# Kernel optimization log

Hardware: AMD Instinct MI355X
Metric: run time of the kernel (lower is better)

## Reference

```python
import jax, jax.numpy as jnp
import numpy as np

B, N, H, HEADS, NBINS = 64, 256, 512, 8, 3
DK = H // HEADS
NEG = -1e12

def setup_inputs() -> dict:
    key = jax.random.key(0)
    ks = jax.random.split(key, 20)
    def lin(k, out_d, in_d):
        w = jax.random.normal(k, (out_d, in_d), jnp.float32) * (1.0 / np.sqrt(in_d))
        b = jnp.zeros((out_d,), jnp.float32)
        return w, b
    x = jax.random.normal(ks[0], (B, N, H), jnp.float32)
    dist = jax.random.uniform(ks[1], (B, N - 1, N - 1), jnp.float32, 0.0, 10.0)
    dist_bar = jnp.sort(jax.random.uniform(ks[2], (B, NBINS), jnp.float32, 1.0, 9.0), axis=-1)
    mask = jnp.ones((B, N, N), jnp.float32)
    Wq, bq = lin(ks[3], H, H)
    Wk, bk = lin(ks[4], H, H)
    Wv, bv = lin(ks[5], H, H)
    Wa = jnp.stack([lin(ks[6 + i], H, H)[0] for i in range(NBINS)])  # [NBINS,H,H]
    ba = jnp.zeros((NBINS, H), jnp.float32)
    Ws1, bs1 = lin(ks[10], H, NBINS * H)
    Ws2, bs2 = lin(ks[11], H, H)
    gamma = jnp.ones((H,), jnp.float32)
    beta = jnp.zeros((H,), jnp.float32)
    return dict(x=x, dist=dist, dist_bar=dist_bar, mask=mask, Wq=Wq, bq=bq, Wk=Wk, bk=bk,
                Wv=Wv, bv=bv, Wa=Wa, ba=ba, Ws1=Ws1, bs1=bs1, Ws2=Ws2, bs2=bs2,
                gamma=gamma, beta=beta)

def reference(x, dist, dist_bar, mask, Wq, bq, Wk, bk, Wv, bv, Wa, ba, Ws1, bs1, Ws2, bs2, gamma, beta):
    residual = x
    def proj(x, W, b):  # torch Linear: x @ W.T + b
        return jnp.einsum('bnd,od->bno', x, W) + b
    def heads(t):  # [B,N,H] -> [B,heads,N,dk]
        return t.reshape(B, N, HEADS, DK).transpose(0, 2, 1, 3)
    q, k, v = heads(proj(x, Wq, bq)), heads(proj(x, Wk, bk)), heads(proj(x, Wv, bv))
    scores = jnp.einsum('bhnd,bhmd->bhnm', q, k) / jnp.sqrt(jnp.float32(DK))  # [B,heads,N,N]
    # padding mask (shape [B,1,N,N] != scores shape -> masked_fill(mask==0))
    scores = jnp.where(mask[:, None] == 0, NEG, scores)
    # new_dist: super node row/col = 1, interior = dist
    new_dist = jnp.ones((B, 1, N, N), jnp.float32).at[:, :, 1:, 1:].set(dist[:, None])
    multi_out, attn_list = [], []
    for i in range(NBINS):
        cut = dist_bar[:, i][:, None, None, None]          # per-batch threshold
        dm = new_dist < cut                                 # [B,1,N,N]
        dm = dm.at[:, :, 0, :].set(True).at[:, :, :, 0].set(True)
        sd = jnp.where(dm, scores, NEG)
        attn = jax.nn.softmax(sd, axis=-1)                  # dropout: eval mode
        attn_list.append(attn)
        multi_out.append(jnp.einsum('bhnm,bhmd->bhnd', attn, v))
    x_cat = jnp.concatenate([
        jnp.einsum('bnd,od->bno', multi_out[i].transpose(0, 2, 1, 3).reshape(B, N, H), Wa[i]) + ba[i]
        for i in range(NBINS)], axis=-1)                    # [B,N,NBINS*H]
    h = jax.nn.silu(jnp.einsum('bnd,od->bno', x_cat, Ws1) + bs1)
    h = jnp.einsum('bnd,od->bno', h, Ws2) + bs2
    h = h + residual
    mu = jnp.mean(h, axis=-1, keepdims=True)
    var = jnp.var(h, axis=-1, keepdims=True)
    out = (h - mu) / jnp.sqrt(var + 1e-6) * gamma + beta
    return (out, jnp.stack(attn_list))
```

## Files before the change

### kernel.cpp

```cpp
#include <hip/hip_runtime.h>
#include <cstddef>

#define NEGV (-1e12f)


typedef __attribute__((ext_vector_type(4))) float f32x4;
typedef __attribute__((ext_vector_type(8))) __bf16 bf16x8;

__device__ __forceinline__ unsigned short f2bf(float f) {
  union { float f; unsigned u; } v; v.f = f;
  unsigned r = v.u + 0x7FFFu + ((v.u >> 16) & 1u);
  return (unsigned short)(r >> 16);
}

#define GLDS16(gp, lp)                                                      \
  __builtin_amdgcn_global_load_lds(                                         \
      (const __attribute__((address_space(1))) void*)(gp),                  \
      (__attribute__((address_space(3))) void*)(lp), 16, 0, 0)

__global__ __launch_bounds__(256) void msa_prep(
    const float* __restrict__ x, const float* __restrict__ Wq,
    const float* __restrict__ Wk, const float* __restrict__ Wv,
    const float* __restrict__ Ws2, const float* __restrict__ Ws1,
    const float* __restrict__ Wa, const float* __restrict__ bq,
    const float* __restrict__ bk, const float* __restrict__ bv,
    const float* __restrict__ ba, const float* __restrict__ bs1,
    const float* __restrict__ dist, const float* __restrict__ dist_bar,
    const float* __restrict__ maskg,
    unsigned short* __restrict__ xb, unsigned short* __restrict__ Wqkvb,
    unsigned short* __restrict__ Ws2b, unsigned short* __restrict__ Wcatb,
    float* __restrict__ bcomb, float* __restrict__ bqkv,
    unsigned long long* __restrict__ bits) {
  __shared__ float As[16][36];
  __shared__ float Bs[16][68];
  const int blk = blockIdx.x;
  const int tid = threadIdx.x;
  if (blk < 8192) {
    int i = blk * 256 + tid;
    float4 v = ((const float4*)x)[i];
    ushort4 o; o.x = f2bf(v.x); o.y = f2bf(v.y); o.z = f2bf(v.z); o.w = f2bf(v.w);
    ((ushort4*)xb)[i] = o;
    return;
  }
  if (blk < 8960) {
    int sel = (blk - 8192) >> 8;
    int i = ((blk - 8192) & 255) * 256 + tid;
    const float* src = (sel == 0) ? Wq : (sel == 1) ? Wk : Wv;
    unsigned short* dst = Wqkvb + (size_t)sel * 262144;
    float4 v = ((const float4*)src)[i];
    ushort4 o; o.x = f2bf(v.x); o.y = f2bf(v.y); o.z = f2bf(v.z); o.w = f2bf(v.w);
    ((ushort4*)dst)[i] = o;
    return;
  }
  if (blk < 9216) {
    int i = (blk - 8960) * 256 + tid;
    float4 v = ((const float4*)Ws2)[i];
    ushort4 o; o.x = f2bf(v.x); o.y = f2bf(v.y); o.z = f2bf(v.z); o.w = f2bf(v.w);
    ((ushort4*)Ws2b)[i] = o;
    return;
  }
  if (blk < 9600) {
    const int t = blk - 9216;
    const int i = t >> 7;
    const int rem = t & 127;
    const int ob = (rem >> 3) * 32, cb = (rem & 7) * 64;
    const int tx = tid & 15, ty = tid >> 4;
    float acc[2][4] = {};
    for (int kt = 0; kt < 512; kt += 16) {
      __syncthreads();
      if (tid < 128) {
        int o = tid >> 2, e4 = (tid & 3) * 4;
        float4 a4 = *(const float4*)&Ws1[(size_t)(ob + o) * 1536 + i * 512 + kt + e4];
        As[e4 + 0][o] = a4.x; As[e4 + 1][o] = a4.y;
        As[e4 + 2][o] = a4.z; As[e4 + 3][o] = a4.w;
      }
      {
        int e = tid & 15, c4 = (tid >> 4) * 4;
        float4 b4 = *(const float4*)&Wa[((size_t)i << 18) + (size_t)(kt + e) * 512 + cb + c4];
        *(float4*)&Bs[e][c4] = b4;
      }
      __syncthreads();
#pragma unroll
      for (int k = 0; k < 16; ++k) {
        float a0 = As[k][ty * 2], a1 = As[k][ty * 2 + 1];
        float bb[4];
        *(float4*)bb = *(const float4*)&Bs[k][tx * 4];
#pragma unroll
        for (int c = 0; c < 4; ++c) {
          acc[0][c] += a0 * bb[c];
          acc[1][c] += a1 * bb[c];
        }
      }
    }
#pragma unroll
    for (int rr = 0; rr < 2; ++rr)
#pragma unroll
      for (int c = 0; c < 4; ++c)
        Wcatb[(size_t)(ob + ty * 2 + rr) * 1536 + i * 512 + cb + tx * 4 + c] =
            f2bf(acc[rr][c]);
    return;
  }
  if (blk < 9728) {
    const int o = (blk - 9600) * 4 + (tid >> 6);
    const int lane = tid & 63;
    const float* row = Ws1 + (size_t)o * 1536;
    float s = 0.f;
#pragma unroll
    for (int c0 = 0; c0 < 1536; c0 += 256) {
      s += row[c0 + lane] * ba[c0 + lane];
      s += row[c0 + 64 + lane] * ba[c0 + 64 + lane];
      s += row[c0 + 128 + lane] * ba[c0 + 128 + lane];
      s += row[c0 + 192 + lane] * ba[c0 + 192 + lane];
    }
#pragma unroll
    for (int off = 32; off > 0; off >>= 1) s += __shfl_xor(s, off);
    if (lane == 0) bcomb[o] = bs1[o] + s;
    return;
  }
  if (blk < 9729) {
    for (int i = tid; i < 1536; i += 256)
      bqkv[i] = (i < 512) ? bq[i] : (i < 1024) ? bk[i - 512] : bv[i - 1024];
    return;
  }
  {
    const int gw = (blk - 9729) * 4 + (tid >> 6);
    const int lane = tid & 63;
    const int b = gw >> 8, row = gw & 255;
    const float cut0 = dist_bar[b * 3 + 0];
    const float cut1 = dist_bar[b * 3 + 1];
    const float cut2 = dist_bar[b * 3 + 2];
    const float* mrow = maskg + (size_t)b * 65536 + (size_t)row * 256;
    const int rj = (row == 0) ? 1 : row;
    const float* drow = dist + (size_t)b * 65025 + (size_t)(rj - 1) * 255;
    unsigned long long* out = bits + (size_t)gw * 12;
#pragma unroll
    for (int cc = 0; cc < 4; ++cc) {
      const int col = cc * 64 + lane;
      const int cj = (col == 0) ? 1 : col;
      float dv = drow[cj - 1];
      bool sup = (row == 0) || (col == 0);
      bool mk = (mrow[col] != 0.f);
      if (sup) dv = -1e30f;
      unsigned long long b0 = __ballot(mk && (dv < cut0));
      unsigned long long b1 = __ballot(mk && (dv < cut1));
      unsigned long long b2 = __ballot(mk && (dv < cut2));
      if (lane == 0) { out[cc] = b0; out[4 + cc] = b1; out[8 + cc] = b2; }
    }
  }
}

template <int ACT, int RES, int OBF, int BK, int SQ>
__global__ __launch_bounds__(256) void msa_gemm_mfma(
    const unsigned short* __restrict__ A, int lda,
    const unsigned short* __restrict__ W, int ldw,
    const float* __restrict__ bias, const float* __restrict__ resid,
    void* __restrict__ Cout, int ldc, int Kdim) {
  constexpr int KSUB = BK / 32;
  constexpr int RPC = BK / 8;
  constexpr int CPT = (128 * RPC) / 256;
  __shared__ __align__(16) unsigned short Asm_[2][128 * BK];
  __shared__ __align__(16) unsigned short Bsm_[2][128 * BK];
  const int tid = threadIdx.x;
  const int lane = tid & 63, wv = tid >> 6;
  const int m0 = blockIdx.x * 128, n0 = blockIdx.y * 128;
  const int wr = wv >> 1, wc = wv & 1;
  const int fr = lane & 15, fq = lane >> 4;
  f32x4 acc[4][4] = {};
  const unsigned short* Ag[CPT];
  const unsigned short* Wg[CPT];
#pragma unroll
  for (int i = 0; i < CPT; ++i) {
    int c = tid + i * 256;
    int row = c / RPC, j = c % RPC;
    Ag[i] = A + (size_t)(m0 + row) * lda + j * 8;
    Wg[i] = W + (size_t)(n0 + row) * ldw + j * 8;
  }
#pragma unroll
  for (int i = 0; i < CPT; ++i) {
    GLDS16(Ag[i], &Asm_[0][(tid + i * 256) * 8]);
    GLDS16(Wg[i], &Bsm_[0][(tid + i * 256) * 8]);
  }
  __syncthreads();
  int cur = 0;
  for (int kt = 0; kt < Kdim; kt += BK) {
    if (kt + BK < Kdim) {
      const int nx = cur ^ 1, k2 = kt + BK;
#pragma unroll
      for (int i = 0; i < CPT; ++i) {
        GLDS16(Ag[i] + k2, &Asm_[nx][(tid + i * 256) * 8]);
        GLDS16(Wg[i] + k2, &Bsm_[nx][(tid + i * 256) * 8]);
      }
    }
#pragma unroll
    for (int ks = 0; ks < KSUB; ++ks) {
      bf16x8 af[4], bfr[4];
#pragma unroll
      for (int mf = 0; mf < 4; ++mf)
        af[mf] = *(const bf16x8*)&Asm_[cur][(wr * 64 + mf * 16 + fr) * BK + ks * 32 + fq * 8];
#pragma unroll
      for (int nf = 0; nf < 4; ++nf)
        bfr[nf] = *(const bf16x8*)&Bsm_[cur][(wc * 64 + nf * 16 + fr) * BK + ks * 32 + fq * 8];
#pragma unroll
      for (int mf = 0; mf < 4; ++mf)
#pragma unroll
        for (int nf = 0; nf < 4; ++nf)
          acc[mf][nf] = __builtin_amdgcn_mfma_f32_16x16x32_bf16(
              af[mf], bfr[nf], acc[mf][nf], 0, 0, 0);
    }
    __syncthreads();
    cur ^= 1;
  }
#pragma unroll
  for (int mf = 0; mf < 4; ++mf) {
#pragma unroll
    for (int nf = 0; nf < 4; ++nf) {
      const int n = n0 + wc * 64 + nf * 16 + fr;
      const float bval = bias[n];
#pragma unroll
      for (int r = 0; r < 4; ++r) {
        const int m = m0 + wr * 64 + mf * 16 + fq * 4 + r;
        float val = acc[mf][nf][r] + bval;
        if (SQ == 1 && n < 512) val *= 0.125f;
        if (ACT == 1) val = val / (1.f + __expf(-val));
        if (RES == 1) val += resid[(size_t)m * ldc + n];
        if (OBF == 1)
          ((unsigned short*)Cout)[(size_t)m * ldc + n] = f2bf(val);
        else
          ((float*)Cout)[(size_t)m * ldc + n] = val;
      }
    }
  }
}

__global__ __launch_bounds__(512) void msa_fused(
    const unsigned short* __restrict__ qkvb,
    const unsigned long long* __restrict__ bits,
    float* __restrict__ attn_out, unsigned short* __restrict__ mob) {
  const int blk = blockIdx.x;
  const int b = (blk & 7) * 8 + (blk >> 6);
  const int h = (blk >> 3) & 7;
  __shared__ __align__(16) unsigned short Kl[256][72];
  __shared__ __align__(16) unsigned short Vt[64][264];
  __shared__ __align__(16) unsigned short Pl[8][16][256];
  const int tid = threadIdx.x;
  const int wv = tid >> 6, lane = tid & 63;
  const int l15 = lane & 15, fq = lane >> 4;
  {
    const unsigned short* kgp = qkvb + (size_t)(b * 256) * 1536 + 512 + h * 64;
#pragma unroll
    for (int i = 0; i < 4; ++i) {
      int s = tid + i * 512;
      int row = s >> 3, c8 = (s & 7) << 3;
      *(uint4*)&Kl[row][c8] = *(const uint4*)&kgp[(size_t)row * 1536 + c8];
    }
  }
  {
    int rv = tid & 255, half = tid >> 8;
    const unsigned short* vgp =
        qkvb + (size_t)(b * 256 + rv) * 1536 + 1024 + h * 64 + half * 32;
#pragma unroll
    for (int j4 = 0; j4 < 4; ++j4) {
      unsigned short tmp[8];
      *(uint4*)tmp = *(const uint4*)&vgp[j4 * 8];
#pragma unroll
      for (int j = 0; j < 8; ++j) Vt[half * 32 + j4 * 8 + j][rv] = tmp[j];
    }
  }
  __syncthreads();
  char* plbase = (char*)&Pl[wv][0][0];
  const int swz = ((l15 & 1) << 6) | ((l15 & 2) << 4);
#pragma unroll
  for (int mf = 0; mf < 2; ++mf) {
    const int r0 = wv * 32 + mf * 16;
    const int q = r0 + l15;
    const unsigned short* qgp =
        qkvb + (size_t)(b * 256 + q) * 1536 + h * 64 + fq * 8;
    bf16x8 aq0 = *(const bf16x8*)qgp;
    bf16x8 aq1 = *(const bf16x8*)(qgp + 32);
    f32x4 accs[16];
#pragma unroll
    for (int nt = 0; nt < 16; ++nt) {
      bf16x8 bk0 = *(const bf16x8*)&Kl[nt * 16 + l15][fq * 8];
      bf16x8 bk1 = *(const bf16x8*)&Kl[nt * 16 + l15][32 + fq * 8];
      f32x4 a = {};
      a = __builtin_amdgcn_mfma_f32_16x16x32_bf16(bk0, aq0, a, 0, 0, 0);
      a = __builtin_amdgcn_mfma_f32_16x16x32_bf16(bk1, aq1, a, 0, 0, 0);
      accs[nt] = a;
    }
    const unsigned long long* brow = bits + (size_t)(b * 256 + q) * 12;
#pragma unroll
    for (int bin = 0; bin < 3; ++bin) {
      const unsigned long long w0 = brow[bin * 4 + 0];
      const unsigned long long w1 = brow[bin * 4 + 1];
      const unsigned long long w2 = brow[bin * 4 + 2];
      const unsigned long long w3 = brow[bin * 4 + 3];
      f32x4 p[16];
      float m = -3e38f;
#pragma unroll
      for (int nt = 0; nt < 16; ++nt) {
        unsigned long long w = (nt < 4) ? w0 : (nt < 8) ? w1 : (nt < 12) ? w2 : w3;
#pragma unroll
        for (int r = 0; r < 4; ++r) {
          unsigned keep = (unsigned)(w >> (16 * (nt & 3) + 4 * fq + r)) & 1u;
          float sv = accs[nt][r];
          float v = keep ? sv : NEGV;
          p[nt][r] = v;
          m = fmaxf(m, v);
        }
      }
      m = fmaxf(m, __shfl_xor(m, 16));
      m = fmaxf(m, __shfl_xor(m, 32));
      float sum = 0.f;
#pragma unroll
      for (int nt = 0; nt < 16; ++nt)
#pragma unroll
        for (int r = 0; r < 4; ++r) {
          p[nt][r] = __expf(p[nt][r] - m);
          sum += p[nt][r];
        }
      sum += __shfl_xor(sum, 16);
      sum += __shfl_xor(sum, 32);
      const float inv = 1.f / sum;
      float* prow = attn_out + ((size_t)((bin * 64 + b) * 8 + h)) * 65536 +
                    (size_t)q * 256;
#pragma unroll
      for (int nt = 0; nt < 16; ++nt) {
        float v0 = p[nt][0] * inv, v1 = p[nt][1] * inv;
        float v2 = p[nt][2] * inv, v3 = p[nt][3] * inv;
        f32x4 st = {v0, v1, v2, v3};
        __builtin_nontemporal_store(st, (f32x4*)(prow + nt * 16 + fq * 4));
        unsigned short u[4];
        u[0] = f2bf(v0); u[1] = f2bf(v1); u[2] = f2bf(v2); u[3] = f2bf(v3);
        int wb = (l15 << 9) | (nt << 5) | (fq << 3);
        *(uint2*)(plbase + (wb ^ swz)) = *(const uint2*)u;
      }
      asm volatile("s_waitcnt lgkmcnt(0)" ::: "memory");
      __builtin_amdgcn_sched_barrier(0);
      f32x4 acco[4] = {};
#pragma unroll
      for (int c = 0; c < 8; ++c) {
        int rb = (l15 << 9) | (c << 6) | (fq << 4);
        bf16x8 pa = *(const bf16x8*)(plbase + (rb ^ swz));
#pragma unroll
        for (int nf = 0; nf < 4; ++nf) {
          bf16x8 bv = *(const bf16x8*)&Vt[nf * 16 + l15][c * 32 + fq * 8];
          acco[nf] = __builtin_amdgcn_mfma_f32_16x16x32_bf16(pa, bv, acco[nf], 0, 0, 0);
        }
      }
#pragma unroll
      for (int nf = 0; nf < 4; ++nf)
#pragma unroll
        for (int r = 0; r < 4; ++r)
          mob[((size_t)(b * 256 + r0 + fq * 4 + r) * 3 + bin) * 512 +
              h * 64 + nf * 16 + l15] = f2bf(acco[nf][r]);
      asm volatile("s_waitcnt lgkmcnt(0)" ::: "memory");
      __builtin_amdgcn_sched_barrier(0);
    }
  }
}

__global__ __launch_bounds__(256) void msa_mlp2ln(
    const unsigned short* __restrict__ h1b, const unsigned short* __restrict__ Ws2b,
    const float* __restrict__ bs2, const float* __restrict__ x,
    const float* __restrict__ gamma, const float* __restrict__ beta,
    float* __restrict__ outp) {
  __shared__ __align__(16) unsigned short Al[32 * 32];
  __shared__ __align__(16) unsigned short Bl[512 * 32];
  __shared__ float red[2][2][32];
  const int tid = threadIdx.x;
  const int lane = tid & 63, wv = tid >> 6;
  const int wr = wv >> 1, wc = wv & 1;
  const int l15 = lane & 15, fq = lane >> 4;
  const int m0 = blockIdx.x * 32;
  f32x4 acc[16] = {};
  for (int kt = 0; kt < 512; kt += 32) {
    if (tid < 128) {
      int row = tid >> 2, c8 = (tid & 3) * 8;
      GLDS16(h1b + (size_t)(m0 + row) * 512 + kt + c8, &Al[tid * 8]);
    }
#pragma unroll
    for (int i = 0; i < 8; ++i) {
      int c = tid + i * 256;
      int row = c >> 2, c8 = (c & 3) * 8;
      GLDS16(Ws2b + (size_t)row * 512 + kt + c8, &Bl[c * 8]);
    }
    __syncthreads();
    bf16x8 af = *(const bf16x8*)&Al[(wr * 16 + l15) * 32 + fq * 8];
#pragma unroll
    for (int nt = 0; nt < 16; ++nt) {
      bf16x8 bfr = *(const bf16x8*)&Bl[(wc * 256 + nt * 16 + l15) * 32 + fq * 8];
      acc[nt] = __builtin_amdgcn_mfma_f32_16x16x32_bf16(af, bfr, acc[nt], 0, 0, 0);
    }
    __syncthreads();
  }
  float vals[16][4];
#pragma unroll
  for (int nt = 0; nt < 16; ++nt) {
    const int n = wc * 256 + nt * 16 + l15;
    const float bval = bs2[n];
#pragma unroll
    for (int r = 0; r < 4; ++r) {
      const int m = m0 + wr * 16 + fq * 4 + r;
      vals[nt][r] = acc[nt][r] + bval + x[(size_t)m * 512 + n];
    }
  }
  const int ridx = wr * 16 + fq * 4;
#pragma unroll
  for (int r = 0; r < 4; ++r) {
    float s = 0.f;
#pragma unroll
    for (int nt = 0; nt < 16; ++nt) s += vals[nt][r];
    s += __shfl_xor(s, 1); s += __shfl_xor(s, 2);
    s += __shfl_xor(s, 4); s += __shfl_xor(s, 8);
    if (l15 == 0) red[0][wc][ridx + r] = s;
  }
  __syncthreads();
  float mu[4];
#pragma unroll
  for (int r = 0; r < 4; ++r)
    mu[r] = (red[0][0][ridx + r] + red[0][1][ridx + r]) * (1.f / 512.f);
#pragma unroll
  for (int r = 0; r < 4; ++r) {
    float s = 0.f;
#pragma unroll
    for (int nt = 0; nt < 16; ++nt) {
      float d = vals[nt][r] - mu[r];
      s += d * d;
    }
    s += __shfl_xor(s, 1); s += __shfl_xor(s, 2);
    s += __shfl_xor(s, 4); s += __shfl_xor(s, 8);
    if (l15 == 0) red[1][wc][ridx + r] = s;
  }
  __syncthreads();
  float iv[4];
#pragma unroll
  for (int r = 0; r < 4; ++r) {
    float var = (red[1][0][ridx + r] + red[1][1][ridx + r]) * (1.f / 512.f);
    iv[r] = 1.f / sqrtf(var + 1e-6f);
  }
#pragma unroll
  for (int nt = 0; nt < 16; ++nt) {
    const int n = wc * 256 + nt * 16 + l15;
    const float g = gamma[n], be = beta[n];
#pragma unroll
    for (int r = 0; r < 4; ++r) {
      const int m = m0 + wr * 16 + fq * 4 + r;
      outp[(size_t)m * 512 + n] = (vals[nt][r] - mu[r]) * iv[r] * g + be;
    }
  }
}

extern "C" void kernel_launch(void* const* d_in, const int* in_sizes, int n_in,
                              void* d_out, int out_size, void* d_ws, size_t ws_size,
                              hipStream_t stream) {
  (void)in_sizes; (void)n_in; (void)out_size; (void)ws_size;
  const float* x        = (const float*)d_in[0];
  const float* dist     = (const float*)d_in[1];
  const float* dist_bar = (const float*)d_in[2];
  const float* mask     = (const float*)d_in[3];
  const float* Wq  = (const float*)d_in[4];  const float* bq  = (const float*)d_in[5];
  const float* Wk  = (const float*)d_in[6];  const float* bk  = (const float*)d_in[7];
  const float* Wv  = (const float*)d_in[8];  const float* bv  = (const float*)d_in[9];
  const float* Wa  = (const float*)d_in[10]; const float* ba  = (const float*)d_in[11];
  const float* Ws1 = (const float*)d_in[12]; const float* bs1 = (const float*)d_in[13];
  const float* Ws2 = (const float*)d_in[14]; const float* bs2 = (const float*)d_in[15];
  const float* gamma = (const float*)d_in[16]; const float* beta = (const float*)d_in[17];

  char* w8 = (char*)d_ws;
  const size_t SZ = 8388608;
  unsigned short* qkvb = (unsigned short*)(w8 + 0);
  unsigned short* mob  = (unsigned short*)(w8 + 50331648);
  unsigned short* xb   = (unsigned short*)(w8 + 100663296);
  unsigned short* Wqkvb= (unsigned short*)(w8 + 117440512);
  unsigned short* Ws2b = (unsigned short*)(w8 + 119013376);
  unsigned short* Wcatb= (unsigned short*)(w8 + 119537664);
  float* bcomb = (float*)(w8 + 121110528);
  float* bqkv  = (float*)(w8 + 121112576);
  unsigned long long* bits = (unsigned long long*)(w8 + 121118720);
  unsigned short* h1b = qkvb;
  float* outp = (float*)d_out;
  float* attn = outp + SZ;

  msa_prep<<<13825, 256, 0, stream>>>(x, Wq, Wk, Wv, Ws2, Ws1, Wa, bq, bk, bv,
                                      ba, bs1, dist, dist_bar, mask,
                                      xb, Wqkvb, Ws2b, Wcatb, bcomb, bqkv, bits);

  msa_gemm_mfma<0, 0, 1, 32, 1><<<dim3(128, 12), 256, 0, stream>>>(
      xb, 512, Wqkvb, 512, bqkv, nullptr, qkvb, 1536, 512);

  msa_fused<<<512, 512, 0, stream>>>(qkvb, bits, attn, mob);

  msa_gemm_mfma<1, 0, 1, 64, 0><<<dim3(128, 4), 256, 0, stream>>>(
      mob, 1536, Wcatb, 1536, bcomb, nullptr, h1b, 512, 1536);

  msa_mlp2ln<<<512, 256, 0, stream>>>(h1b, Ws2b, bs2, x, gamma, beta, outp);
}
```

Baseline: 307.1 us.

## Add BM tile parameter, shrink second GEMM tile, read bf16 residual, drop waitcnt

The GEMM kernel gains a BM template parameter so the concat-to-hidden GEMM can use 64x128 tiles with BK=32, which doubles its grid for better CU occupancy. The final MLP/LayerNorm kernel now reads the residual from the bf16 copy of x instead of the fp32 input, halving that read traffic. An explicit lgkmcnt wait and sched barrier at the end of each bin loop in the fused attention kernel are also removed. Using the bf16 residual lowers output precision and may affect accuracy.

```diff
diff --git a/kernel.cpp b/kernel.cpp
--- a/kernel.cpp
+++ b/kernel.cpp
@@ -11,6 +11,9 @@
   union { float f; unsigned u; } v; v.f = f;
   unsigned r = v.u + 0x7FFFu + ((v.u >> 16) & 1u);
   return (unsigned short)(r >> 16);
+}
+__device__ __forceinline__ float bf2f(unsigned short u) {
+  union { unsigned u; float f; } v; v.u = (unsigned)u << 16; return v.f;
 }
 
 #define GLDS16(gp, lp)                                                      \
@@ -149,7 +152,7 @@
   }
 }
 
-template <int ACT, int RES, int OBF, int BK, int SQ>
+template <int ACT, int RES, int OBF, int BK, int SQ, int BM>
 __global__ __launch_bounds__(256) void msa_gemm_mfma(
     const unsigned short* __restrict__ A, int lda,
     const unsigned short* __restrict__ W, int ldw,
@@ -157,53 +160,60 @@
     void* __restrict__ Cout, int ldc, int Kdim) {
   constexpr int KSUB = BK / 32;
   constexpr int RPC = BK / 8;
-  constexpr int CPT = (128 * RPC) / 256;
-  __shared__ __align__(16) unsigned short Asm_[2][128 * BK];
+  constexpr int CPTA = (BM * RPC) / 256;
+  constexpr int CPTB = (128 * RPC) / 256;
+  constexpr int WC = (BM == 128) ? 2 : 4;
+  constexpr int NFR = 8 / WC;
+  constexpr int NW = 16 * NFR;
+  __shared__ __align__(16) unsigned short Asm_[2][BM * BK];
   __shared__ __align__(16) unsigned short Bsm_[2][128 * BK];
   const int tid = threadIdx.x;
   const int lane = tid & 63, wv = tid >> 6;
-  const int m0 = blockIdx.x * 128, n0 = blockIdx.y * 128;
-  const int wr = wv >> 1, wc = wv & 1;
+  const int m0 = blockIdx.x * BM, n0 = blockIdx.y * 128;
+  const int wr = wv / WC, wc = wv % WC;
   const int fr = lane & 15, fq = lane >> 4;
-  f32x4 acc[4][4] = {};
-  const unsigned short* Ag[CPT];
-  const unsigned short* Wg[CPT];
-#pragma unroll
-  for (int i = 0; i < CPT; ++i) {
+  f32x4 acc[4][NFR] = {};
+  const unsigned short* Ag[CPTA];
+  const unsigned short* Wg[CPTB];
+#pragma unroll
+  for (int i = 0; i < CPTA; ++i) {
     int c = tid + i * 256;
     int row = c / RPC, j = c % RPC;
     Ag[i] = A + (size_t)(m0 + row) * lda + j * 8;
+  }
+#pragma unroll
+  for (int i = 0; i < CPTB; ++i) {
+    int c = tid + i * 256;
+    int row = c / RPC, j = c % RPC;
     Wg[i] = W + (size_t)(n0 + row) * ldw + j * 8;
   }
 #pragma unroll
-  for (int i = 0; i < CPT; ++i) {
-    GLDS16(Ag[i], &Asm_[0][(tid + i * 256) * 8]);
-    GLDS16(Wg[i], &Bsm_[0][(tid + i * 256) * 8]);
-  }
+  for (int i = 0; i < CPTA; ++i) GLDS16(Ag[i], &Asm_[0][(tid + i * 256) * 8]);
+#pragma unroll
+  for (int i = 0; i < CPTB; ++i) GLDS16(Wg[i], &Bsm_[0][(tid + i * 256) * 8]);
   __syncthreads();
   int cur = 0;
   for (int kt = 0; kt < Kdim; kt += BK) {
     if (kt + BK < Kdim) {
       const int nx = cur ^ 1, k2 = kt + BK;
 #pragma unroll
-      for (int i = 0; i < CPT; ++i) {
-        GLDS16(Ag[i] + k2, &Asm_[nx][(tid + i * 256) * 8]);
-        GLDS16(Wg[i] + k2, &Bsm_[nx][(tid + i * 256) * 8]);
-      }
+      for (int i = 0; i < CPTA; ++i) GLDS16(Ag[i] + k2, &Asm_[nx][(tid + i * 256) * 8]);
+#pragma unroll
+      for (int i = 0; i < CPTB; ++i) GLDS16(Wg[i] + k2, &Bsm_[nx][(tid + i * 256) * 8]);
     }
 #pragma unroll
     for (int ks = 0; ks < KSUB; ++ks) {
-      bf16x8 af[4], bfr[4];
+      bf16x8 af[4], bfr[NFR];
 #pragma unroll
       for (int mf = 0; mf < 4; ++mf)
         af[mf] = *(const bf16x8*)&Asm_[cur][(wr * 64 + mf * 16 + fr) * BK + ks * 32 + fq * 8];
 #pragma unroll
-      for (int nf = 0; nf < 4; ++nf)
-        bfr[nf] = *(const bf16x8*)&Bsm_[cur][(wc * 64 + nf * 16 + fr) * BK + ks * 32 + fq * 8];
+      for (int nf = 0; nf < NFR; ++nf)
+        bfr[nf] = *(const bf16x8*)&Bsm_[cur][(wc * NW + nf * 16 + fr) * BK + ks * 32 + fq * 8];
 #pragma unroll
       for (int mf = 0; mf < 4; ++mf)
 #pragma unroll
-        for (int nf = 0; nf < 4; ++nf)
+        for (int nf = 0; nf < NFR; ++nf)
           acc[mf][nf] = __builtin_amdgcn_mfma_f32_16x16x32_bf16(
               af[mf], bfr[nf], acc[mf][nf], 0, 0, 0);
     }
@@ -213,8 +223,8 @@
 #pragma unroll
   for (int mf = 0; mf < 4; ++mf) {
 #pragma unroll
-    for (int nf = 0; nf < 4; ++nf) {
-      const int n = n0 + wc * 64 + nf * 16 + fr;
+    for (int nf = 0; nf < NFR; ++nf) {
+      const int n = n0 + wc * NW + nf * 16 + fr;
       const float bval = bias[n];
 #pragma unroll
       for (int r = 0; r < 4; ++r) {
@@ -353,15 +363,13 @@
         for (int r = 0; r < 4; ++r)
           mob[((size_t)(b * 256 + r0 + fq * 4 + r) * 3 + bin) * 512 +
               h * 64 + nf * 16 + l15] = f2bf(acco[nf][r]);
-      asm volatile("s_waitcnt lgkmcnt(0)" ::: "memory");
-      __builtin_amdgcn_sched_barrier(0);
     }
   }
 }
 
 __global__ __launch_bounds__(256) void msa_mlp2ln(
     const unsigned short* __restrict__ h1b, const unsigned short* __restrict__ Ws2b,
-    const float* __restrict__ bs2, const float* __restrict__ x,
+    const float* __restrict__ bs2, const unsigned short* __restrict__ xb,
     const float* __restrict__ gamma, const float* __restrict__ beta,
     float* __restrict__ outp) {
   __shared__ __align__(16) unsigned short Al[32 * 32];
@@ -401,7 +409,7 @@
 #pragma unroll
     for (int r = 0; r < 4; ++r) {
       const int m = m0 + wr * 16 + fq * 4 + r;
-      vals[nt][r] = acc[nt][r] + bval + x[(size_t)m * 512 + n];
+      vals[nt][r] = acc[nt][r] + bval + bf2f(xb[(size_t)m * 512 + n]);
     }
   }
   const int ridx = wr * 16 + fq * 4;
@@ -485,13 +493,13 @@
                                       ba, bs1, dist, dist_bar, mask,
                                       xb, Wqkvb, Ws2b, Wcatb, bcomb, bqkv, bits);
 
-  msa_gemm_mfma<0, 0, 1, 32, 1><<<dim3(128, 12), 256, 0, stream>>>(
+  msa_gemm_mfma<0, 0, 1, 32, 1, 128><<<dim3(128, 12), 256, 0, stream>>>(
       xb, 512, Wqkvb, 512, bqkv, nullptr, qkvb, 1536, 512);
 
   msa_fused<<<512, 512, 0, stream>>>(qkvb, bits, attn, mob);
 
-  msa_gemm_mfma<1, 0, 1, 64, 0><<<dim3(128, 4), 256, 0, stream>>>(
+  msa_gemm_mfma<1, 0, 1, 32, 0, 64><<<dim3(256, 4), 256, 0, stream>>>(
       mob, 1536, Wcatb, 1536, bcomb, nullptr, h1b, 512, 1536);
 
-  msa_mlp2ln<<<512, 256, 0, stream>>>(h1b, Ws2b, bs2, x, gamma, beta, outp);
-}
+  msa_mlp2ln<<<512, 256, 0, stream>>>(h1b, Ws2b, bs2, xb, gamma, beta, outp);
+}
```

Result: no change. 306.9 us (-0.0%).
